# Kernel tuning notes

Hardware: AMD Instinct MI355X
Metric: run time of the kernel (lower is better)

## Reference

```python
import jax, jax.numpy as jnp
import numpy as np

BLOCK_SIZE = 64
HIDDEN = 1024
INTERMEDIATE = 4096
NUM_BLOCK = HIDDEN // BLOCK_SIZE              # 16
INT_BLOCK = (INTERMEDIATE // HIDDEN) * BLOCK_SIZE  # 256


def setup_inputs() -> dict:
    key = jax.random.key(0)
    k_x, k_w1, k_b1, k_w2, k_b2 = jax.random.split(key, 5)
    hidden_states = jax.random.normal(k_x, (4, 2048, HIDDEN), dtype=jnp.float32)
    w1 = 0.02 * jax.random.normal(k_w1, (NUM_BLOCK, INT_BLOCK, BLOCK_SIZE), dtype=jnp.float32)
    b1 = 0.001 * jax.random.normal(k_b1, (INTERMEDIATE,), dtype=jnp.float32)
    w2 = 0.02 * jax.random.normal(k_w2, (NUM_BLOCK, BLOCK_SIZE, INT_BLOCK), dtype=jnp.float32)
    b2 = 0.001 * jax.random.normal(k_b2, (HIDDEN,), dtype=jnp.float32)
    return {"hidden_states": hidden_states, "w1": w1, "b1": b1, "w2": w2, "b2": b2}


def reference(hidden_states, w1, b1, w2, b2):
    lead = hidden_states.shape[:-1]
    dim = hidden_states.shape[-1]
    nb, ibs, bs = w1.shape  # num_block, intermediate_block_size, block_size
    x = hidden_states.reshape(-1, nb, bs)                 # [B, n, i]
    h = jnp.einsum('bni,noi->bno', x, w1)                 # [B, n, o]
    # channel shuffle: transpose block and feature axes before flattening
    h = jnp.swapaxes(h, -1, -2).reshape(-1, nb * ibs)     # [B, o*n order]
    h = jax.nn.gelu(h + b1, approximate=False)
    h = h.reshape(-1, nb, ibs)                            # regroup after shuffle
    y = jnp.einsum('bni,noi->bno', h, w2).reshape(-1, nb * bs) + b2
    return y.reshape(*lead, dim)
```

## Files before the change

### kernel.cpp

```cpp
#include <hip/hip_runtime.h>
#include <hip/hip_bf16.h>


typedef __attribute__((ext_vector_type(8))) short  short8;
typedef __attribute__((ext_vector_type(4))) short  short4v;
typedef __attribute__((ext_vector_type(4))) float  floatx4;

__device__ __forceinline__ short f2bf(float f) {
  union { __hip_bfloat16 h; short s; } u;
  u.h = __float2bfloat16(f);
  return u.s;
}
__device__ __forceinline__ float bf2f(short s) {
  union { float f; unsigned u; } uu;
  uu.u = ((unsigned)(unsigned short)s) << 16;
  return uu.f;
}

__device__ __forceinline__ float gelu_f(float v) {
  float v2 = v * v;
  float p  = fmaf(0.044715f, v2, 1.0f);
  float t  = v * p;
  float e  = __builtin_amdgcn_exp2f(-2.3020807f * t);
  return v * __builtin_amdgcn_rcpf(1.0f + e);
}

__global__ void pack_k(const float* __restrict__ w1, const float* __restrict__ w2,
                       const float* __restrict__ b1, short* __restrict__ w1p,
                       short* __restrict__ w2p, short* __restrict__ b1p) {
  const int t = blockIdx.x * blockDim.x + threadIdx.x;
  const int lane = t & 63;
  const int lhi = lane >> 4;
  if (t < 32768) {
    const int ks = (t >> 6) & 1, np = (t >> 7) & 15, n = (t >> 11) & 15;
    const float* src = w1 + ((size_t)(n * 256 + np * 16 + (lane & 15)) * 64 + ks * 32 + lhi * 8);
    short8 f;
#pragma unroll
    for (int e = 0; e < 8; ++e) f[e] = f2bf(src[e]);
    *(short8*)(w1p + (size_t)t * 8) = f;
  } else if (t < 65536) {
    const int t2 = t - 32768;
    const int ot = (t2 >> 6) & 3, ks = (t2 >> 8) & 7, np = (t2 >> 11) & 15;
    const int op = ot * 16 + (lane & 15);
    short8 f;
#pragma unroll
    for (int e = 0; e < 8; ++e) {
      const int k = ks * 32 + lhi * 8 + e;
      f[e] = f2bf(w2[(size_t)(np * 64 + op) * 256 + (k & 15) * 16 + (k >> 4)]);
    }
    *(short8*)(w2p + (size_t)t2 * 8) = f;
  } else {
    const int t3 = t - 65536;
    const int np = (t3 >> 6) & 15, n = (t3 >> 10) & 15;
    short4v b;
#pragma unroll
    for (int r = 0; r < 4; ++r) b[r] = f2bf(b1[(np * 16 + lhi * 4 + r) * 16 + n]);
    *(short4v*)(b1p + (size_t)((n * 16 + np) * 64 + lane) * 4) = b;
  }
}

__global__ __launch_bounds__(256, 3) void k1_gemm1(
    const float* __restrict__ x, const short* __restrict__ w1p,
    const short* __restrict__ b1p, short* __restrict__ G) {
  const int tid = threadIdx.x;
  const int wv = tid >> 6, lane = tid & 63;
  const int l15 = lane & 15, lhi = lane >> 4;
  const int b   = blockIdx.x;
  const int rtg = b & 127;
  const int n   = ((b >> 7) << 1) | (wv >> 1);
  const int np0 = (wv & 1) * 8;

  short8  wf[8][2];
  short4v bv[8];
#pragma unroll
  for (int j = 0; j < 8; ++j) {
    const int np = np0 + j;
    wf[j][0] = *(const short8*)(w1p + (size_t)(((n * 16 + np) * 2 + 0) * 64 + lane) * 8);
    wf[j][1] = *(const short8*)(w1p + (size_t)(((n * 16 + np) * 2 + 1) * 64 + lane) * 8);
    bv[j]    = *(const short4v*)(b1p + (size_t)((n * 16 + np) * 64 + lane) * 4);
  }

#pragma unroll
  for (int r = 0; r < 4; ++r) {
    const int rt = rtg * 4 + r;
    const float* px = x + (size_t)(rt * 16 + l15) * 1024 + n * 64 + lhi * 8;
    floatx4 a0 = *(const floatx4*)px;
    floatx4 a1 = *(const floatx4*)(px + 4);
    floatx4 a2 = *(const floatx4*)(px + 32);
    floatx4 a3 = *(const floatx4*)(px + 36);
    short8 xf0, xf1;
#pragma unroll
    for (int e = 0; e < 4; ++e) {
      xf0[e] = f2bf(a0[e]); xf0[e + 4] = f2bf(a1[e]);
      xf1[e] = f2bf(a2[e]); xf1[e + 4] = f2bf(a3[e]);
    }
    short* gb = G + (size_t)rt * 65536 + n * 256 + l15 * 16 + lhi * 4;
#pragma unroll
    for (int j = 0; j < 8; ++j) {
      floatx4 acc = {0.f, 0.f, 0.f, 0.f};
      acc = __builtin_amdgcn_mfma_f32_16x16x32_bf16(wf[j][0], xf0, acc, 0, 0, 0);
      acc = __builtin_amdgcn_mfma_f32_16x16x32_bf16(wf[j][1], xf1, acc, 0, 0, 0);
      short4v hv;
#pragma unroll
      for (int e = 0; e < 4; ++e)
        hv[e] = f2bf(gelu_f(acc[e] + bf2f(bv[j][e])));
      *(short4v*)(gb + (size_t)(np0 + j) * 4096) = hv;
    }
  }
}

__global__ __launch_bounds__(256, 4) void k2_gemm2(
    const short* __restrict__ G, const short* __restrict__ w2p,
    const float* __restrict__ b2, float* __restrict__ y) {
  const int tid = threadIdx.x;
  const int wv = tid >> 6, lane = tid & 63;
  const int l15 = lane & 15, lhi = lane >> 4;
  const int rt = blockIdx.x >> 2;
  const int np = (blockIdx.x & 3) * 4 + wv;

  const short* ab = G + (size_t)(rt * 16 + np) * 4096 + (lhi >> 1) * 256 + l15 * 16 + (lhi & 1) * 8;
  short8 af[8];
#pragma unroll
  for (int ks = 0; ks < 8; ++ks)
    af[ks] = *(const short8*)(ab + ks * 512);

#pragma unroll
  for (int ot = 0; ot < 4; ++ot) {
    floatx4 a0 = {0.f, 0.f, 0.f, 0.f}, a1 = {0.f, 0.f, 0.f, 0.f};
#pragma unroll
    for (int ks = 0; ks < 8; ks += 2) {
      short8 b0  = *(const short8*)(w2p + (size_t)(((np * 8 + ks) * 4 + ot) * 64 + lane) * 8);
      short8 b1f = *(const short8*)(w2p + (size_t)(((np * 8 + ks + 1) * 4 + ot) * 64 + lane) * 8);
      a0 = __builtin_amdgcn_mfma_f32_16x16x32_bf16(af[ks], b0, a0, 0, 0, 0);
      a1 = __builtin_amdgcn_mfma_f32_16x16x32_bf16(af[ks + 1], b1f, a1, 0, 0, 0);
    }
    const int col = np * 64 + ot * 16 + l15;
    const float bb = b2[col];
    float* py = y + (size_t)(rt * 16 + lhi * 4) * 1024 + col;
#pragma unroll
    for (int r = 0; r < 4; ++r)
      py[(size_t)r * 1024] = a0[r] + a1[r] + bb;
  }
}

extern "C" void kernel_launch(void* const* d_in, const int* in_sizes, int n_in,
                              void* d_out, int out_size, void* d_ws, size_t ws_size,
                              hipStream_t stream) {
  const float* x  = (const float*)d_in[0];
  const float* w1 = (const float*)d_in[1];
  const float* b1 = (const float*)d_in[2];
  const float* w2 = (const float*)d_in[3];
  const float* b2 = (const float*)d_in[4];
  float* y = (float*)d_out;

  short* w1p = (short*)d_ws;
  short* w2p = w1p + 16 * 256 * 64;
  short* b1p = w2p + 16 * 256 * 64;
  short* G   = b1p + 16 * 16 * 64 * 4;

  pack_k<<<160, 512, 0, stream>>>(w1, w2, b1, w1p, w2p, b1p);
  k1_gemm1<<<1024, 256, 0, stream>>>(x, w1p, b1p, G);
  k2_gemm2<<<2048, 256, 0, stream>>>(G, w2p, b2, y);
}
```

Before: 50.45 us.

## Restructure gemm1 work split and double-buffer x loads across row tiles

Each block in the first GEMM now owns one input block and eight row tiles, and each wave handles four output sub-tiles instead of eight. This roughly halves the per-wave weight registers, and launch bounds are raised to allow four blocks per CU. The x loads are software-pipelined with two register buffers so the next row tile's global loads are in flight while the current one runs MFMA and GELU. The GELU polynomial is also folded into one fma. Costs are higher register pressure from the double buffers and each x tile now being loaded by all four waves of a block.

```diff
diff --git a/kernel.cpp b/kernel.cpp
--- a/kernel.cpp
+++ b/kernel.cpp
@@ -18,10 +18,10 @@
 }
 
 __device__ __forceinline__ float gelu_f(float v) {
-  float v2 = v * v;
-  float p  = fmaf(0.044715f, v2, 1.0f);
-  float t  = v * p;
-  float e  = __builtin_amdgcn_exp2f(-2.3020807f * t);
+  float m = v * v;
+  float c = fmaf(-0.1029375f, m, -2.3020807f);
+  float z = v * c;
+  float e = __builtin_amdgcn_exp2f(z);
   return v * __builtin_amdgcn_rcpf(1.0f + e);
 }
 
@@ -59,54 +59,72 @@
   }
 }
 
-__global__ __launch_bounds__(256, 3) void k1_gemm1(
+__global__ __launch_bounds__(256, 4) void k1_gemm1(
     const float* __restrict__ x, const short* __restrict__ w1p,
     const short* __restrict__ b1p, short* __restrict__ G) {
   const int tid = threadIdx.x;
   const int wv = tid >> 6, lane = tid & 63;
   const int l15 = lane & 15, lhi = lane >> 4;
   const int b   = blockIdx.x;
-  const int rtg = b & 127;
-  const int n   = ((b >> 7) << 1) | (wv >> 1);
-  const int np0 = (wv & 1) * 8;
+  const int n   = b >> 6;
+  const int rtg = b & 63;
+  const int np0 = wv * 4;
 
-  short8  wf[8][2];
-  short4v bv[8];
+  short8  wf[4][2];
+  short4v bv[4];
 #pragma unroll
-  for (int j = 0; j < 8; ++j) {
+  for (int j = 0; j < 4; ++j) {
     const int np = np0 + j;
     wf[j][0] = *(const short8*)(w1p + (size_t)(((n * 16 + np) * 2 + 0) * 64 + lane) * 8);
     wf[j][1] = *(const short8*)(w1p + (size_t)(((n * 16 + np) * 2 + 1) * 64 + lane) * 8);
     bv[j]    = *(const short4v*)(b1p + (size_t)((n * 16 + np) * 64 + lane) * 4);
   }
 
+  const float* xb = x + (size_t)(rtg * 8 * 16 + l15) * 1024 + n * 64 + lhi * 8;
+  const size_t rstep = (size_t)16 * 1024;
+
+#define XLOAD(B0, B1, B2, B3, r)                      \
+  {                                                   \
+    const float* px_ = xb + (size_t)(r) * rstep;      \
+    B0 = *(const floatx4*)px_;                        \
+    B1 = *(const floatx4*)(px_ + 4);                  \
+    B2 = *(const floatx4*)(px_ + 32);                 \
+    B3 = *(const floatx4*)(px_ + 36);                 \
+  }
+
+#define COMPUTE(B0, B1, B2, B3, r)                                            \
+  {                                                                           \
+    short8 xf0, xf1;                                                          \
+    _Pragma("unroll")                                                         \
+    for (int e = 0; e < 4; ++e) {                                             \
+      xf0[e] = f2bf(B0[e]); xf0[e + 4] = f2bf(B1[e]);                         \
+      xf1[e] = f2bf(B2[e]); xf1[e + 4] = f2bf(B3[e]);                         \
+    }                                                                         \
+    short* gb_ = G + (size_t)(rtg * 8 + (r)) * 65536 + n * 256 + l15 * 16 + lhi * 4; \
+    _Pragma("unroll")                                                         \
+    for (int j = 0; j < 4; ++j) {                                             \
+      floatx4 acc = {0.f, 0.f, 0.f, 0.f};                                     \
+      acc = __builtin_amdgcn_mfma_f32_16x16x32_bf16(wf[j][0], xf0, acc, 0, 0, 0); \
+      acc = __builtin_amdgcn_mfma_f32_16x16x32_bf16(wf[j][1], xf1, acc, 0, 0, 0); \
+      short4v hv;                                                             \
+      _Pragma("unroll")                                                       \
+      for (int e = 0; e < 4; ++e)                                             \
+        hv[e] = f2bf(gelu_f(acc[e] + bf2f(bv[j][e])));                        \
+      *(short4v*)(gb_ + (size_t)(np0 + j) * 4096) = hv;                       \
+    }                                                                         \
+  }
+
+  floatx4 A0, A1, A2, A3, B0, B1, B2, B3;
+  XLOAD(A0, A1, A2, A3, 0)
 #pragma unroll
-  for (int r = 0; r < 4; ++r) {
-    const int rt = rtg * 4 + r;
-    const float* px = x + (size_t)(rt * 16 + l15) * 1024 + n * 64 + lhi * 8;
-    floatx4 a0 = *(const floatx4*)px;
-    floatx4 a1 = *(const floatx4*)(px + 4);
-    floatx4 a2 = *(const floatx4*)(px + 32);
-    floatx4 a3 = *(const floatx4*)(px + 36);
-    short8 xf0, xf1;
-#pragma unroll
-    for (int e = 0; e < 4; ++e) {
-      xf0[e] = f2bf(a0[e]); xf0[e + 4] = f2bf(a1[e]);
-      xf1[e] = f2bf(a2[e]); xf1[e + 4] = f2bf(a3[e]);
-    }
-    short* gb = G + (size_t)rt * 65536 + n * 256 + l15 * 16 + lhi * 4;
-#pragma unroll
-    for (int j = 0; j < 8; ++j) {
-      floatx4 acc = {0.f, 0.f, 0.f, 0.f};
-      acc = __builtin_amdgcn_mfma_f32_16x16x32_bf16(wf[j][0], xf0, acc, 0, 0, 0);
-      acc = __builtin_amdgcn_mfma_f32_16x16x32_bf16(wf[j][1], xf1, acc, 0, 0, 0);
-      short4v hv;
-#pragma unroll
-      for (int e = 0; e < 4; ++e)
-        hv[e] = f2bf(gelu_f(acc[e] + bf2f(bv[j][e])));
-      *(short4v*)(gb + (size_t)(np0 + j) * 4096) = hv;
-    }
+  for (int rp = 0; rp < 4; ++rp) {
+    XLOAD(B0, B1, B2, B3, rp * 2 + 1)
+    COMPUTE(A0, A1, A2, A3, rp * 2)
+    if (rp < 3) XLOAD(A0, A1, A2, A3, rp * 2 + 2)
+    COMPUTE(B0, B1, B2, B3, rp * 2 + 1)
   }
+#undef XLOAD
+#undef COMPUTE
 }
 
 __global__ __launch_bounds__(256, 4) void k2_gemm2(
```

Measured after the change: 52.20 us. 3.5% more time.

## Stage x tile in LDS with coalesced loads and share it across four waves

Applied to the files above, without the earlier changes.

k1 now has each block stage a 128-row by 64-column slice of x into shared memory as bf16, using coalesced float4 loads. All four waves reuse that slice, and each wave covers 4 np groups instead of 8. Previously every wave loaded and converted x rows itself with strided loads. The change also raises the occupancy hint to 4 and folds the GELU polynomial constants to save a multiply. The costs are LDS usage, a barrier, and a different block-to-work mapping that must still cover all rows and n.

```diff
diff --git a/kernel.cpp b/kernel.cpp
--- a/kernel.cpp
+++ b/kernel.cpp
@@ -5,6 +5,8 @@
 typedef __attribute__((ext_vector_type(8))) short  short8;
 typedef __attribute__((ext_vector_type(4))) short  short4v;
 typedef __attribute__((ext_vector_type(4))) float  floatx4;
+
+#define XPITCH 72
 
 __device__ __forceinline__ short f2bf(float f) {
   union { __hip_bfloat16 h; short s; } u;
@@ -18,10 +20,10 @@
 }
 
 __device__ __forceinline__ float gelu_f(float v) {
-  float v2 = v * v;
-  float p  = fmaf(0.044715f, v2, 1.0f);
-  float t  = v * p;
-  float e  = __builtin_amdgcn_exp2f(-2.3020807f * t);
+  float m = v * v;
+  float c = fmaf(-0.1029375f, m, -2.3020807f);
+  float z = v * c;
+  float e = __builtin_amdgcn_exp2f(z);
   return v * __builtin_amdgcn_rcpf(1.0f + e);
 }
 
@@ -59,44 +61,52 @@
   }
 }
 
-__global__ __launch_bounds__(256, 3) void k1_gemm1(
+__global__ __launch_bounds__(256, 4) void k1_gemm1(
     const float* __restrict__ x, const short* __restrict__ w1p,
     const short* __restrict__ b1p, short* __restrict__ G) {
+  __shared__ __align__(16) short xs[128 * XPITCH];
+
   const int tid = threadIdx.x;
   const int wv = tid >> 6, lane = tid & 63;
   const int l15 = lane & 15, lhi = lane >> 4;
   const int b   = blockIdx.x;
-  const int rtg = b & 127;
-  const int n   = ((b >> 7) << 1) | (wv >> 1);
-  const int np0 = (wv & 1) * 8;
+  const int n   = b >> 6;
+  const int rtg = b & 63;
+  const int np0 = wv * 4;
 
-  short8  wf[8][2];
-  short4v bv[8];
+  short8  wf[4][2];
+  short4v bv[4];
 #pragma unroll
-  for (int j = 0; j < 8; ++j) {
+  for (int j = 0; j < 4; ++j) {
     const int np = np0 + j;
     wf[j][0] = *(const short8*)(w1p + (size_t)(((n * 16 + np) * 2 + 0) * 64 + lane) * 8);
     wf[j][1] = *(const short8*)(w1p + (size_t)(((n * 16 + np) * 2 + 1) * 64 + lane) * 8);
     bv[j]    = *(const short4v*)(b1p + (size_t)((n * 16 + np) * 64 + lane) * 4);
   }
 
+  {
+    const int rr = tid >> 4;
+    const int cc = (tid & 15) * 4;
+    const float* px = x + (size_t)(rtg * 128 + rr) * 1024 + n * 64 + cc;
 #pragma unroll
-  for (int r = 0; r < 4; ++r) {
-    const int rt = rtg * 4 + r;
-    const float* px = x + (size_t)(rt * 16 + l15) * 1024 + n * 64 + lhi * 8;
-    floatx4 a0 = *(const floatx4*)px;
-    floatx4 a1 = *(const floatx4*)(px + 4);
-    floatx4 a2 = *(const floatx4*)(px + 32);
-    floatx4 a3 = *(const floatx4*)(px + 36);
-    short8 xf0, xf1;
+    for (int p = 0; p < 8; ++p) {
+      floatx4 v = *(const floatx4*)(px + (size_t)p * 16 * 1024);
+      short4v s;
 #pragma unroll
-    for (int e = 0; e < 4; ++e) {
-      xf0[e] = f2bf(a0[e]); xf0[e + 4] = f2bf(a1[e]);
-      xf1[e] = f2bf(a2[e]); xf1[e + 4] = f2bf(a3[e]);
+      for (int e = 0; e < 4; ++e) s[e] = f2bf(v[e]);
+      *(short4v*)(&xs[(p * 16 + rr) * XPITCH + cc]) = s;
     }
-    short* gb = G + (size_t)rt * 65536 + n * 256 + l15 * 16 + lhi * 4;
+  }
+  __syncthreads();
+
 #pragma unroll
-    for (int j = 0; j < 8; ++j) {
+  for (int rt = 0; rt < 8; ++rt) {
+    const short* xrow = &xs[(rt * 16 + l15) * XPITCH];
+    short8 xf0 = *(const short8*)(xrow + lhi * 8);
+    short8 xf1 = *(const short8*)(xrow + 32 + lhi * 8);
+    short* gb = G + (size_t)(rtg * 8 + rt) * 65536 + n * 256 + l15 * 16 + lhi * 4;
+#pragma unroll
+    for (int j = 0; j < 4; ++j) {
       floatx4 acc = {0.f, 0.f, 0.f, 0.f};
       acc = __builtin_amdgcn_mfma_f32_16x16x32_bf16(wf[j][0], xf0, acc, 0, 0, 0);
       acc = __builtin_amdgcn_mfma_f32_16x16x32_bf16(wf[j][1], xf1, acc, 0, 0, 0);
```

After: 49.36 us. 1.02x faster.
